# Kernel tuning notes

Measured on AMD Instinct MI355X. Metric: run time of the kernel, lower is better.

The kernel has to match this reference:

```python
import jax, jax.numpy as jnp
import numpy as np

HEADS = 8
DIM_HEAD = 64
SCALE = DIM_HEAD ** -0.5


def setup_inputs() -> dict:
    key = jax.random.key(0)
    k1, k2, k3 = jax.random.split(key, 3)
    b, p, n, dim = 2, 16, 512, 512
    inner = HEADS * DIM_HEAD  # 512
    x = jax.random.normal(k1, (b, p, n, dim), dtype=jnp.float32)
    W_qkv = jax.random.normal(k2, (dim, 3 * inner), dtype=jnp.float32) * (dim ** -0.5)
    W_out = jax.random.normal(k3, (inner, dim), dtype=jnp.float32) * (inner ** -0.5)
    b_out = jnp.zeros((dim,), dtype=jnp.float32)
    return {"x": x, "W_qkv": W_qkv, "W_out": W_out, "b_out": b_out}


def reference(x, W_qkv, W_out, b_out):
    b, p, n, dim = x.shape
    # QKV projection (no bias), split into q, k, v
    qkv = jnp.einsum('bpnd,de->bpne', x, W_qkv)
    q, k, v = jnp.split(qkv, 3, axis=-1)
    # (b, p, n, h*d) -> (b, p, h, n, d)
    def to_heads(t):
        return t.reshape(b, p, n, HEADS, DIM_HEAD).transpose(0, 1, 3, 2, 4)
    q, k, v = to_heads(q), to_heads(k), to_heads(v)
    # attention scores: (b, p, h, n, n)
    dots = jnp.einsum('bphnd,bphmd->bphnm', q, k) * SCALE
    attn = jax.nn.softmax(dots, axis=-1)
    out = jnp.einsum('bphnm,bphmd->bphnd', attn, v)
    # (b, p, h, n, d) -> (b, p, n, h*d)
    out = out.transpose(0, 1, 3, 2, 4).reshape(b, p, n, HEADS * DIM_HEAD)
    # output projection (dropout rate = 0.0 -> identity)
    return jnp.einsum('bpne,ed->bpnd', out, W_out) + b_out
```

## Files before the change

### kernel.cpp

```cpp
#include <hip/hip_runtime.h>
#include <hip/hip_bf16.h>

typedef short bf16x8 __attribute__((ext_vector_type(8)));
typedef short bf16x4 __attribute__((ext_vector_type(4)));
typedef float f32x4  __attribute__((ext_vector_type(4)));
typedef float f32x16 __attribute__((ext_vector_type(16)));

__device__ __forceinline__ unsigned short f2bf(float f) {
    union { float fv; unsigned int u; } v; v.fv = f;
    unsigned int r = v.u + 0x7FFFu + ((v.u >> 16) & 1u);
    return (unsigned short)(r >> 16);
}

__device__ __forceinline__ short f2bf_n(float f) {
    union { __hip_bfloat16 h; short s; } u;
    u.h = __float2bfloat16(f);
    return u.s;
}

__device__ __forceinline__ unsigned int cvtpk(float lo, float hi) {
    unsigned int r;
    asm volatile("v_cvt_pk_bf16_f32 %0, %1, %2" : "=v"(r) : "v"(lo), "v"(hi));
    return r;
}

__device__ __forceinline__ void gload16(const short* g, short* l) {
    __builtin_amdgcn_global_load_lds(
        (const __attribute__((address_space(1))) void*)g,
        (__attribute__((address_space(3))) void*)l, 16, 0, 0);
}

__global__ __launch_bounds__(256) void prep_all(
    const float* __restrict__ x, short* __restrict__ xb,
    const float* __restrict__ Wqkv, const float* __restrict__ Wout,
    short* __restrict__ Wqkvt, short* __restrict__ Woutt)
{
    if (blockIdx.x < 4096) {
        size_t i = ((size_t)blockIdx.x * 256 + threadIdx.x) * 8;
        f32x4 a = *(const f32x4*)(x + i);
        f32x4 b = *(const f32x4*)(x + i + 4);
        bf16x8 s;
        #pragma unroll
        for (int e = 0; e < 4; ++e) { s[e] = (short)f2bf(a[e]); s[4 + e] = (short)f2bf(b[e]); }
        *(bf16x8*)(xb + i) = s;
        return;
    }
    __shared__ float tile[32][33];
    const int b = blockIdx.x - 4096;
    const float* src; short* dst; int N, bb;
    if (b < 768) { src = Wqkv; dst = Wqkvt; N = 1536; bb = b; }
    else         { src = Wout; dst = Woutt; N = 512;  bb = b - 768; }
    const int tx = threadIdx.x;
    const int nb = N >> 5;
    const int k0 = (bb / nb) * 32;
    const int n0 = (bb % nb) * 32;
    const int r  = tx >> 3;
    const int c4 = (tx & 7) * 4;
    f32x4 v = *(const f32x4*)(src + (size_t)(k0 + r) * N + n0 + c4);
    #pragma unroll
    for (int e = 0; e < 4; ++e) tile[r][c4 + e] = v[e];
    __syncthreads();
    bf16x4 o;
    #pragma unroll
    for (int e = 0; e < 4; ++e) o[e] = (short)f2bf(tile[c4 + e][r]);
    *(bf16x4*)(dst + (size_t)(n0 + r) * 512 + k0 + c4) = o;
}

template<int F32OUT>
__global__ __launch_bounds__(256, 2) void gemm_db(
    const short* __restrict__ A, const short* __restrict__ Bt,
    short* __restrict__ Cb, float* __restrict__ Cf, const float* __restrict__ bias,
    int M, int N, int K, int NB)
{
    __shared__ short lds[2][2][128 * 64];
    const int t    = threadIdx.x;
    const int lane = t & 63;
    const int wid  = t >> 6;
    const int l15  = lane & 15;
    const int lg   = lane >> 4;

    const int cpx = gridDim.x >> 3;
    const int swz = (blockIdx.x & 7) * cpx + (blockIdx.x >> 3);
    const int m0 = (swz / NB) * 128;
    const int n0 = (swz % NB) * 128;

    const int wm = (wid >> 1) * 64;
    const int wn = (wid & 1) * 64;

    const int scol = 8 * ((lane & 7) ^ ((lane >> 3) & 7));

    float bval[4];
    if constexpr (F32OUT) {
        #pragma unroll
        for (int ni = 0; ni < 4; ++ni) bval[ni] = bias[n0 + wn + ni * 16 + l15];
    }

    f32x4 acc[4][4];
    #pragma unroll
    for (int i = 0; i < 4; ++i)
        #pragma unroll
        for (int j = 0; j < 4; ++j)
            acc[i][j] = f32x4{0.f, 0.f, 0.f, 0.f};

    const int NT = K >> 6;

    auto stage = [&](int buf, int tk) {
        #pragma unroll
        for (int j = 0; j < 4; ++j) {
            const int r = wid * 32 + j * 8 + (lane >> 3);
            gload16(A  + (size_t)(m0 + r) * K + tk * 64 + scol,
                    &lds[buf][0][(wid * 32 + j * 8) * 64]);
            gload16(Bt + (size_t)(n0 + r) * K + tk * 64 + scol,
                    &lds[buf][1][(wid * 32 + j * 8) * 64]);
        }
    };

    stage(0, 0);

    for (int tk = 0; tk < NT; ++tk) {
        const int cur = tk & 1;
        if (tk + 1 < NT) {
            stage(cur ^ 1, tk + 1);
            asm volatile("s_waitcnt vmcnt(8)" ::: "memory");
        } else {
            asm volatile("s_waitcnt vmcnt(0)" ::: "memory");
        }
        __builtin_amdgcn_s_barrier();

        bf16x8 af[4][2], bg[4][2];
        #pragma unroll
        for (int kk = 0; kk < 2; ++kk) {
            #pragma unroll
            for (int mi = 0; mi < 4; ++mi)
                af[mi][kk] = *(const bf16x8*)&lds[cur][0][
                    (wm + mi * 16 + l15) * 64 + (((kk * 4 + lg) ^ (l15 & 7)) * 8)];
            #pragma unroll
            for (int ni = 0; ni < 4; ++ni)
                bg[ni][kk] = *(const bf16x8*)&lds[cur][1][
                    (wn + ni * 16 + l15) * 64 + (((kk * 4 + lg) ^ (l15 & 7)) * 8)];
        }

        __builtin_amdgcn_s_setprio(1);
        #pragma unroll
        for (int kk = 0; kk < 2; ++kk)
            #pragma unroll
            for (int mi = 0; mi < 4; ++mi)
                #pragma unroll
                for (int ni = 0; ni < 4; ++ni)
                    acc[mi][ni] = __builtin_amdgcn_mfma_f32_16x16x32_bf16(
                        af[mi][kk], bg[ni][kk], acc[mi][ni], 0, 0, 0);
        __builtin_amdgcn_s_setprio(0);
        __builtin_amdgcn_s_barrier();
    }

    #pragma unroll
    for (int mi = 0; mi < 4; ++mi) {
        #pragma unroll
        for (int ni = 0; ni < 4; ++ni) {
            const int col = n0 + wn + ni * 16 + l15;
            #pragma unroll
            for (int r = 0; r < 4; ++r) {
                const int rowi = m0 + wm + mi * 16 + 4 * lg + r;
                if constexpr (F32OUT) {
                    Cf[(size_t)rowi * N + col] = acc[mi][ni][r] + bval[ni];
                } else {
                    Cb[(size_t)rowi * N + col] = (short)f2bf(acc[mi][ni][r]);
                }
            }
        }
    }
}

__global__ __launch_bounds__(512, 4) void attn_kernel(
    const short* __restrict__ qkv, short* __restrict__ attn_out)
{
    __shared__ short Kl[2][4096];
    __shared__ short Vt[2][5120];
    const int t    = threadIdx.x;
    const int lane = t & 63;
    const int wid  = t >> 6;
    const int l31  = lane & 31;
    const int hi   = lane >> 5;
    const int pairid = blockIdx.x & 255;
    const int qh  = blockIdx.x >> 8;
    const int bp  = pairid >> 3;
    const int h   = pairid & 7;
    const size_t tok0 = (size_t)bp * 512;
    const int q0   = qh * 256 + wid * 32;
    const int qcol = h * 64;

    bf16x8 qf[4];
    #pragma unroll
    for (int kf = 0; kf < 4; ++kf)
        qf[kf] = *(const bf16x8*)(qkv + (tok0 + q0 + l31) * 1536
                                  + qcol + kf * 16 + 8 * hi);

    f32x16 ot0, ot1;
    #pragma unroll
    for (int r = 0; r < 16; ++r) { ot0[r] = 0.f; ot1[r] = 0.f; }
    float mrun = -1e30f, lrun = 0.f;

    const int krow = t >> 3;
    const short* Ksrc0 = qkv + (tok0 + krow) * 1536 + 512 + qcol
                         + 8 * ((t & 7) ^ (krow & 7));
    const int sn = t >> 3;
    const int sd = (t & 7) * 8;
    const short* Vsrc0 = qkv + (tok0 + sn) * 1536 + 1024 + qcol + sd;
    const int kvp = (sn & 7) | (((sn >> 3) ^ (t & 7)) << 3);

    gload16(Ksrc0, &Kl[0][t * 8]);
    bf16x8 vreg = *(const bf16x8*)(Vsrc0);

    const float C = 0.18033688011112042f;

    for (int tkv = 0; tkv < 8; ++tkv) {
        const int cur = tkv & 1;
        #pragma unroll
        for (int i = 0; i < 8; ++i)
            Vt[cur][(sd + i) * 80 + kvp] = vreg[i];
        __syncthreads();
        if (tkv < 7) {
            gload16(Ksrc0 + (size_t)(tkv + 1) * 64 * 1536, &Kl[cur ^ 1][t * 8]);
            vreg = *(const bf16x8*)(Vsrc0 + (size_t)(tkv + 1) * 64 * 1536);
        }

        f32x16 st0, st1;
        #pragma unroll
        for (int r = 0; r < 16; ++r) { st0[r] = 0.f; st1[r] = 0.f; }
        __builtin_amdgcn_s_setprio(1);
        #pragma unroll
        for (int kf = 0; kf < 4; ++kf) {
            const int slot = ((2 * kf + hi) ^ (l31 & 7)) * 8;
            bf16x8 k0 = *(const bf16x8*)&Kl[cur][l31 * 64 + slot];
            bf16x8 k1 = *(const bf16x8*)&Kl[cur][(32 + l31) * 64 + slot];
            st0 = __builtin_amdgcn_mfma_f32_32x32x16_bf16(k0, qf[kf], st0, 0, 0, 0);
            st1 = __builtin_amdgcn_mfma_f32_32x32x16_bf16(k1, qf[kf], st1, 0, 0, 0);
        }
        __builtin_amdgcn_s_setprio(0);

        float pm = st0[0];
        #pragma unroll
        for (int r = 1; r < 16; ++r) pm = fmaxf(pm, st0[r]);
        #pragma unroll
        for (int r = 0; r < 16; ++r) pm = fmaxf(pm, st1[r]);
        pm = fmaxf(pm, __shfl_xor(pm, 32));
        pm *= C;
        if (!__all(pm <= mrun + 8.f)) {
            const float mnew = fmaxf(mrun, pm);
            const float fsc  = __builtin_amdgcn_exp2f(mrun - mnew);
            lrun *= fsc;
            #pragma unroll
            for (int r = 0; r < 16; ++r) { ot0[r] *= fsc; ot1[r] *= fsc; }
            mrun = mnew;
        }
        float ps = 0.f;
        #pragma unroll
        for (int r = 0; r < 16; ++r) {
            st0[r] = __builtin_amdgcn_exp2f(__builtin_fmaf(st0[r], C, -mrun));
            ps += st0[r];
        }
        #pragma unroll
        for (int r = 0; r < 16; ++r) {
            st1[r] = __builtin_amdgcn_exp2f(__builtin_fmaf(st1[r], C, -mrun));
            ps += st1[r];
        }
        ps += __shfl_xor(ps, 32);
        lrun += ps;

        __builtin_amdgcn_s_setprio(1);
#define PVKS(KS, ST)                                                          \
        {                                                                     \
            const int a8 = ((KS) & 1) * 8;                                    \
            unsigned int s0a = cvtpk(ST[a8 + 0], ST[a8 + 1]);                 \
            unsigned int s0b = cvtpk(ST[a8 + 2], ST[a8 + 3]);                 \
            unsigned int s1a = cvtpk(ST[a8 + 4], ST[a8 + 5]);                 \
            unsigned int s1b = cvtpk(ST[a8 + 6], ST[a8 + 7]);                 \
            asm volatile("v_permlane32_swap_b32 %0, %1"                       \
                         : "+v"(s0a), "+v"(s1a));                             \
            asm volatile("v_permlane32_swap_b32 %0, %1"                       \
                         : "+v"(s0b), "+v"(s1b));                             \
            union { unsigned int w[4]; bf16x8 v; } pu;                        \
            pu.w[0] = s0a; pu.w[1] = s0b; pu.w[2] = s1a; pu.w[3] = s1b;       \
            {                                                                 \
                const int sl0 = ((2 * (KS) + hi) ^ (l31 >> 3)) * 8;           \
                bf16x8 vf = *(const bf16x8*)&Vt[cur][l31 * 80 + sl0];         \
                ot0 = __builtin_amdgcn_mfma_f32_32x32x16_bf16(                \
                    vf, pu.v, ot0, 0, 0, 0);                                  \
            }                                                                 \
            {                                                                 \
                const int sl1 = ((2 * (KS) + hi) ^ (4 ^ (l31 >> 3))) * 8;     \
                bf16x8 vf = *(const bf16x8*)&Vt[cur][(32 + l31) * 80 + sl1];  \
                ot1 = __builtin_amdgcn_mfma_f32_32x32x16_bf16(                \
                    vf, pu.v, ot1, 0, 0, 0);                                  \
            }                                                                 \
        }
        PVKS(0, st0)
        PVKS(1, st0)
        PVKS(2, st1)
        PVKS(3, st1)
#undef PVKS
        __builtin_amdgcn_s_setprio(0);
    }

    const float inv = 1.f / lrun;
    short* obase = attn_out + (tok0 + q0 + l31) * 512 + qcol + 4 * hi;
    #pragma unroll
    for (int rq = 0; rq < 4; ++rq) {
        bf16x4 o0, o1;
        #pragma unroll
        for (int j = 0; j < 4; ++j) {
            o0[j] = f2bf_n(ot0[4 * rq + j] * inv);
            o1[j] = f2bf_n(ot1[4 * rq + j] * inv);
        }
        *(bf16x4*)(obase + rq * 8)      = o0;
        *(bf16x4*)(obase + 32 + rq * 8) = o1;
    }
}

extern "C" void kernel_launch(void* const* d_in, const int* in_sizes, int n_in,
                              void* d_out, int out_size, void* d_ws, size_t ws_size,
                              hipStream_t stream) {
    const float* x    = (const float*)d_in[0];
    const float* Wqkv = (const float*)d_in[1];
    const float* Wout = (const float*)d_in[2];
    const float* bout = (const float*)d_in[3];
    float* out = (float*)d_out;

    char* ws = (char*)d_ws;
    short* qkvb  = (short*)(ws);
    short* xb    = (short*)(ws + 50331648ull);
    short* attnb = xb;
    short* Wqkvt = (short*)(ws + 67108864ull);
    short* Woutt = (short*)(ws + 68681728ull);

    prep_all<<<5120, 256, 0, stream>>>(x, xb, Wqkv, Wout, Wqkvt, Woutt);

    gemm_db<0><<<1536, 256, 0, stream>>>(xb, Wqkvt, qkvb, nullptr, nullptr,
                                         16384, 1536, 512, 12);

    attn_kernel<<<512, 512, 0, stream>>>(qkvb, attnb);

    gemm_db<1><<<512, 256, 0, stream>>>(attnb, Woutt, nullptr, out, bout,
                                        16384, 512, 512, 4);
}
```

Before: 91.80 us.

## Fuse fp32-to-bf16 conversion of x into the QKV GEMM A-tile load

The separate pass that converted x to bf16 is removed, and a new QKV GEMM kernel reads fp32 x directly into registers, converts it to bf16 and writes it into LDS itself. B is still staged with direct global-to-LDS loads. This drops a 32MB fp32 read plus a 16MB bf16 write and read round trip, but each of the 12 N-blocks now rereads the fp32 A rows, which doubles A traffic from L2/HBM. It also adds register pressure and VALU conversion work inside the GEMM pipeline.

```diff
diff --git a/kernel.cpp b/kernel.cpp
--- a/kernel.cpp
+++ b/kernel.cpp
@@ -30,23 +30,12 @@
         (__attribute__((address_space(3))) void*)l, 16, 0, 0);
 }
 
-__global__ __launch_bounds__(256) void prep_all(
-    const float* __restrict__ x, short* __restrict__ xb,
+__global__ __launch_bounds__(256) void tr_w2(
     const float* __restrict__ Wqkv, const float* __restrict__ Wout,
     short* __restrict__ Wqkvt, short* __restrict__ Woutt)
 {
-    if (blockIdx.x < 4096) {
-        size_t i = ((size_t)blockIdx.x * 256 + threadIdx.x) * 8;
-        f32x4 a = *(const f32x4*)(x + i);
-        f32x4 b = *(const f32x4*)(x + i + 4);
-        bf16x8 s;
-        #pragma unroll
-        for (int e = 0; e < 4; ++e) { s[e] = (short)f2bf(a[e]); s[4 + e] = (short)f2bf(b[e]); }
-        *(bf16x8*)(xb + i) = s;
-        return;
-    }
     __shared__ float tile[32][33];
-    const int b = blockIdx.x - 4096;
+    const int b = blockIdx.x;
     const float* src; short* dst; int N, bb;
     if (b < 768) { src = Wqkv; dst = Wqkvt; N = 1536; bb = b; }
     else         { src = Wout; dst = Woutt; N = 512;  bb = b - 768; }
@@ -64,6 +53,128 @@
     #pragma unroll
     for (int e = 0; e < 4; ++e) o[e] = (short)f2bf(tile[c4 + e][r]);
     *(bf16x4*)(dst + (size_t)(n0 + r) * 512 + k0 + c4) = o;
+}
+
+__global__ __launch_bounds__(256, 2) void gemm_f32a(
+    const float* __restrict__ A, const short* __restrict__ Bt,
+    short* __restrict__ Cb, int M, int N, int K, int NB)
+{
+    __shared__ short lds[2][2][128 * 64];
+    const int t    = threadIdx.x;
+    const int lane = t & 63;
+    const int wid  = t >> 6;
+    const int l15  = lane & 15;
+    const int lg   = lane >> 4;
+
+    const int cpx = gridDim.x >> 3;
+    const int swz = (blockIdx.x & 7) * cpx + (blockIdx.x >> 3);
+    const int m0 = (swz / NB) * 128;
+    const int n0 = (swz % NB) * 128;
+
+    const int wm = (wid >> 1) * 64;
+    const int wn = (wid & 1) * 64;
+
+    const int srow = lane >> 3;
+    const int scol = 8 * ((lane & 7) ^ ((lane >> 3) & 7));
+
+    f32x4 acc[4][4];
+    #pragma unroll
+    for (int i = 0; i < 4; ++i)
+        #pragma unroll
+        for (int j = 0; j < 4; ++j)
+            acc[i][j] = f32x4{0.f, 0.f, 0.f, 0.f};
+
+    f32x4 areg[4][2];
+
+    const int NT = K >> 6;
+
+    auto loadA = [&](int tk) {
+        #pragma unroll
+        for (int j = 0; j < 4; ++j) {
+            const float* src = A + (size_t)(m0 + wid * 32 + j * 8 + srow) * K
+                               + tk * 64 + scol;
+            areg[j][0] = *(const f32x4*)src;
+            areg[j][1] = *(const f32x4*)(src + 4);
+        }
+    };
+    auto writeA = [&](int buf) {
+        #pragma unroll
+        for (int j = 0; j < 4; ++j) {
+            bf16x8 s;
+            #pragma unroll
+            for (int e = 0; e < 4; ++e) {
+                s[e]     = (short)f2bf(areg[j][0][e]);
+                s[4 + e] = (short)f2bf(areg[j][1][e]);
+            }
+            *(bf16x8*)&lds[buf][0][(wid * 32 + j * 8 + srow) * 64 + (lane & 7) * 8] = s;
+        }
+    };
+    auto stageB = [&](int buf, int tk) {
+        #pragma unroll
+        for (int j = 0; j < 4; ++j)
+            gload16(Bt + (size_t)(n0 + wid * 32 + j * 8 + srow) * K + tk * 64 + scol,
+                    &lds[buf][1][(wid * 32 + j * 8) * 64]);
+    };
+
+    loadA(0);
+    stageB(0, 0);
+    asm volatile("s_waitcnt vmcnt(4)" ::: "memory");
+    writeA(0);
+    loadA(1);
+    asm volatile("s_waitcnt vmcnt(8) lgkmcnt(0)" ::: "memory");
+    __builtin_amdgcn_s_barrier();
+
+    for (int tk = 0; tk < NT; ++tk) {
+        const int cur = tk & 1;
+        if (tk + 1 < NT) {
+            asm volatile("s_waitcnt vmcnt(0)" ::: "memory");
+            writeA(cur ^ 1);
+            stageB(cur ^ 1, tk + 1);
+            if (tk + 2 < NT) loadA(tk + 2);
+            asm volatile("s_waitcnt lgkmcnt(0)" ::: "memory");
+        } else {
+            asm volatile("s_waitcnt vmcnt(0)" ::: "memory");
+        }
+        __builtin_amdgcn_s_barrier();
+
+        bf16x8 af[4][2], bg[4][2];
+        #pragma unroll
+        for (int kk = 0; kk < 2; ++kk) {
+            #pragma unroll
+            for (int mi = 0; mi < 4; ++mi)
+                af[mi][kk] = *(const bf16x8*)&lds[cur][0][
+                    (wm + mi * 16 + l15) * 64 + (((kk * 4 + lg) ^ (l15 & 7)) * 8)];
+            #pragma unroll
+            for (int ni = 0; ni < 4; ++ni)
+                bg[ni][kk] = *(const bf16x8*)&lds[cur][1][
+                    (wn + ni * 16 + l15) * 64 + (((kk * 4 + lg) ^ (l15 & 7)) * 8)];
+        }
+
+        __builtin_amdgcn_s_setprio(1);
+        #pragma unroll
+        for (int kk = 0; kk < 2; ++kk)
+            #pragma unroll
+            for (int mi = 0; mi < 4; ++mi)
+                #pragma unroll
+                for (int ni = 0; ni < 4; ++ni)
+                    acc[mi][ni] = __builtin_amdgcn_mfma_f32_16x16x32_bf16(
+                        af[mi][kk], bg[ni][kk], acc[mi][ni], 0, 0, 0);
+        __builtin_amdgcn_s_setprio(0);
+        __builtin_amdgcn_s_barrier();
+    }
+
+    #pragma unroll
+    for (int mi = 0; mi < 4; ++mi) {
+        #pragma unroll
+        for (int ni = 0; ni < 4; ++ni) {
+            const int col = n0 + wn + ni * 16 + l15;
+            #pragma unroll
+            for (int r = 0; r < 4; ++r) {
+                const int rowi = m0 + wm + mi * 16 + 4 * lg + r;
+                Cb[(size_t)rowi * N + col] = (short)f2bf(acc[mi][ni][r]);
+            }
+        }
+    }
 }
 
 template<int F32OUT>
@@ -328,15 +439,13 @@
 
     char* ws = (char*)d_ws;
     short* qkvb  = (short*)(ws);
-    short* xb    = (short*)(ws + 50331648ull);
-    short* attnb = xb;
+    short* attnb = (short*)(ws + 50331648ull);
     short* Wqkvt = (short*)(ws + 67108864ull);
     short* Woutt = (short*)(ws + 68681728ull);
 
-    prep_all<<<5120, 256, 0, stream>>>(x, xb, Wqkv, Wout, Wqkvt, Woutt);
-
-    gemm_db<0><<<1536, 256, 0, stream>>>(xb, Wqkvt, qkvb, nullptr, nullptr,
-                                         16384, 1536, 512, 12);
+    tr_w2<<<1024, 256, 0, stream>>>(Wqkv, Wout, Wqkvt, Woutt);
+
+    gemm_f32a<<<1536, 256, 0, stream>>>(x, Wqkvt, qkvb, 16384, 1536, 512, 12);
 
     attn_kernel<<<512, 512, 0, stream>>>(qkvb, attnb);
 
```

Measured after the change: 102.9 us. +12.1%, slower.
